# Kernel optimization log

Measured on AMD Instinct MI355X. Metric: run time of the kernel, lower is better.

## Reference

```python
import jax, jax.numpy as jnp
import numpy as np
from jax.scipy.special import ndtr

EPS1 = 1e-6
WEIGHT_DECAY = 1e-5  # FLAGS.weight_decay


def setup_inputs() -> dict:
    key = jax.random.key(0)
    ks = jax.random.split(key, 12)
    B, F, C, Z, S = 512, 512, 500, 64, 100  # batch, features, classes (r_dim), z_dim, n_sample
    lim = np.sqrt(6.0 / (C + Z))
    def glorot(k, shape):
        fan_in, fan_out = shape
        s = np.sqrt(2.0 / (fan_in + fan_out))
        return jax.random.normal(k, shape, jnp.float32) * s
    return {
        "input_X": jax.random.normal(ks[0], (B, F), jnp.float32),
        "input_Y": (jax.random.uniform(ks[1], (B, C)) < 0.1).astype(jnp.float32),  # multi-label targets
        "noise": jax.random.normal(ks[2], (S, B, Z), jnp.float32),
        "W1": glorot(ks[3], (F, 128)), "b1": jnp.zeros((128,), jnp.float32),
        "W2": glorot(ks[4], (128, 256)), "b2": jnp.zeros((256,), jnp.float32),
        "W3": glorot(ks[5], (256, 256)), "b3": jnp.zeros((256,), jnp.float32),
        "Wmu": glorot(ks[6], (256, C)), "bmu": jnp.zeros((C,), jnp.float32),
        "r_sqrt_sigma": jax.random.uniform(ks[7], (C, Z), jnp.float32, -lim, lim),
    }


def reference(input_X, input_Y, noise, W1, b1, W2, b2, W3, b3, Wmu, bmu, r_sqrt_sigma):
    # MLP trunk
    h = jax.nn.relu(input_X @ W1 + b1)
    h = jax.nn.relu(h @ W2 + b2)
    feature = jax.nn.relu(h @ W3 + b3)

    # low-rank covariance: sigma = R R^T, covariance = sigma + I
    cov_diag = jnp.sum(r_sqrt_sigma * r_sqrt_sigma, axis=1) + 1.0  # [C]

    normalized_mu = feature @ Wmu + bmu            # [B, C]
    r_mu = normalized_mu * jnp.sqrt(cov_diag)      # [B, C]

    # MC samples of latent r: [S, B, C]
    sample_r = jnp.einsum('sbz,cz->sbc', noise, r_sqrt_sigma) + r_mu

    E = ndtr(sample_r) * (1.0 - EPS1) + EPS1 * 0.5  # probit CDF, clamped
    # logprob = sum_c [ Y*log(E) + (1-Y)*log(1-E) ]  (== -sum sample_nll)
    logprob = jnp.sum(jnp.log(E) * input_Y + jnp.log1p(-E) * (1.0 - input_Y), axis=2)  # [S, B]
    maxlogprob = jnp.max(logprob, axis=0)                       # [B]
    Eprob = jnp.mean(jnp.exp(logprob - maxlogprob), axis=0)     # [B]
    nll_loss = jnp.mean(-jnp.log(Eprob) - maxlogprob)

    # marginal (independent) probit approximated by scaled sigmoid
    indiv_prob = jax.nn.sigmoid(normalized_mu * 1.70169) * (1.0 - EPS1) + 0.5 * EPS1
    cross_entropy = jnp.log(indiv_prob) * input_Y + jnp.log1p(-indiv_prob) * (1.0 - input_Y)
    marginal_loss = -jnp.mean(jnp.sum(cross_entropy, axis=1))

    l2_loss = WEIGHT_DECAY * (jnp.sum(W1 * W1) + jnp.sum(W2 * W2)
                              + jnp.sum(W3 * W3) + jnp.sum(Wmu * Wmu))
    total_loss = l2_loss + nll_loss
    return indiv_prob, nll_loss, marginal_loss, l2_loss, total_loss
```

## Files before the change

### kernel.cpp

```cpp
#include <hip/hip_runtime.h>
#include <cstddef>

#define EPS1f 1e-6f
#define WDf   1e-5f

constexpr int Bsz = 512, Csz = 500, Zsz = 64, Ssz = 100;

typedef short bf16x8 __attribute__((ext_vector_type(8)));
typedef float f32x4 __attribute__((ext_vector_type(4)));

__device__ inline short f2bf(float f) {
  union { float f; unsigned u; } v; v.f = f;
  unsigned r = (v.u + 0x7fffu + ((v.u >> 16) & 1u)) >> 16;
  return (short)r;
}

__device__ inline float log_probit(float t) {
  const float u = t * -0.70710678118654752f;
  const float au = fabsf(u);
  const float s = 1.f / fmaf(0.3275911f, au, 1.f);
  float p = fmaf(1.061405429f, s, -1.453152027f);
  p = fmaf(p, s, 1.421413741f);
  p = fmaf(p, s, -0.284496736f);
  p = fmaf(p, s, 0.254829592f);
  p = p * s;
  const float e = __expf(-au * au);
  const float f = p * e;
  const float erfc_u = (u < 0.f) ? (2.f - f) : f;
  const float E = fmaf(0.5f * erfc_u, 1.f - EPS1f, 0.5f * EPS1f);
  return __logf(E);
}

__device__ inline float block_reduce_sum(float v, float* red) {
  #pragma unroll
  for (int off = 32; off > 0; off >>= 1) v += __shfl_down(v, off, 64);
  const int lane = threadIdx.x & 63, wid = threadIdx.x >> 6;
  if (lane == 0) red[wid] = v;
  __syncthreads();
  float r = 0.f;
  if (threadIdx.x == 0) {
    const int nw = blockDim.x >> 6;
    for (int i = 0; i < nw; ++i) r += red[i];
  }
  __syncthreads();
  return r;
}

__device__ __forceinline__ void gemm32_body(
    const float* __restrict__ A, const float* __restrict__ W,
    const float* __restrict__ bias, float* __restrict__ out,
    int M, int N, int K, int bn0, int bm0, float* As_, float* Ws_, bool relu) {
  const int tid = threadIdx.x;
  const int bn = bn0 * 32, bm = bm0 * 32;
  const int sm = tid >> 3, sk4 = (tid & 7) * 4;
  const int sk = tid >> 3, sn4 = (tid & 7) * 4;
  const int tn = tid & 15, tm = tid >> 4;
  #define AS_(b, k, m) As_[(b) * 1152 + (k) * 36 + (m)]
  #define WS_(b, k, n) Ws_[(b) * 1152 + (k) * 36 + (n)]
  auto loadW = [&](int kt, float4& wv) {
    const float* wrow = W + (size_t)(kt + sk) * N;
    const int nn = bn + sn4;
    if (nn + 3 < N) wv = *reinterpret_cast<const float4*>(wrow + nn);
    else {
      wv.x = (nn + 0 < N) ? wrow[nn + 0] : 0.f;
      wv.y = (nn + 1 < N) ? wrow[nn + 1] : 0.f;
      wv.z = (nn + 2 < N) ? wrow[nn + 2] : 0.f;
      wv.w = (nn + 3 < N) ? wrow[nn + 3] : 0.f;
    }
  };
  {
    float4 av = *reinterpret_cast<const float4*>(A + (size_t)(bm + sm) * K + sk4);
    float4 wv; loadW(0, wv);
    AS_(0, sk4 + 0, sm) = av.x; AS_(0, sk4 + 1, sm) = av.y;
    AS_(0, sk4 + 2, sm) = av.z; AS_(0, sk4 + 3, sm) = av.w;
    *reinterpret_cast<float4*>(&WS_(0, sk, sn4)) = wv;
  }
  __syncthreads();
  float acc[2][2] = {};
  int pb = 0;
  for (int kt = 0; kt < K; kt += 32) {
    const bool more = (kt + 32) < K;
    float4 av2, wv2;
    if (more) {
      av2 = *reinterpret_cast<const float4*>(A + (size_t)(bm + sm) * K + kt + 32 + sk4);
      loadW(kt + 32, wv2);
    }
    #pragma unroll
    for (int k = 0; k < 32; ++k) {
      const float2 a = *reinterpret_cast<const float2*>(&AS_(pb, k, tm * 2));
      const float2 w = *reinterpret_cast<const float2*>(&WS_(pb, k, tn * 2));
      acc[0][0] = fmaf(a.x, w.x, acc[0][0]);
      acc[0][1] = fmaf(a.x, w.y, acc[0][1]);
      acc[1][0] = fmaf(a.y, w.x, acc[1][0]);
      acc[1][1] = fmaf(a.y, w.y, acc[1][1]);
    }
    if (more) {
      const int nb = pb ^ 1;
      AS_(nb, sk4 + 0, sm) = av2.x; AS_(nb, sk4 + 1, sm) = av2.y;
      AS_(nb, sk4 + 2, sm) = av2.z; AS_(nb, sk4 + 3, sm) = av2.w;
      *reinterpret_cast<float4*>(&WS_(nb, sk, sn4)) = wv2;
      __syncthreads();
      pb = nb;
    }
  }
  #pragma unroll
  for (int j = 0; j < 2; ++j) {
    const int n = bn + tn * 2 + j;
    if (n >= N) continue;
    const float bv = bias[n];
    #pragma unroll
    for (int i = 0; i < 2; ++i) {
      const int m = bm + tm * 2 + i;
      float v = acc[i][j] + bv;
      if (relu) v = fmaxf(v, 0.f);
      out[(size_t)m * N + n] = v;
    }
  }
  #undef AS_
  #undef WS_
}

__global__ __launch_bounds__(256) void prep_kernel(
    const float* __restrict__ noise, short* __restrict__ nfB,
    const float* __restrict__ R, short* __restrict__ Rb, float* __restrict__ sqrtcov,
    const float* __restrict__ X, const float* __restrict__ W1,
    const float* __restrict__ b1, float* __restrict__ h1,
    const float* __restrict__ W2, const float* __restrict__ W3,
    const float* __restrict__ Wmu, float* __restrict__ l2_part) {
  __shared__ float smem[2304 * 2];
  const int blk = blockIdx.x;
  const int tid = threadIdx.x;
  if (blk < 800) {
    const int g = blk * 256 + tid;
    const int s = g >> 11;
    const int r = g & 2047;
    const int bt = r >> 6;
    const int ln = r & 63;
    const int cl = ln & 15, grp = ln >> 4;
    const float* src = noise + ((size_t)(s * 512 + bt * 16 + cl) * 64 + grp * 8);
    const float4 a = *reinterpret_cast<const float4*>(src);
    const float4 b = *reinterpret_cast<const float4*>(src + 4);
    const float4 c = *reinterpret_cast<const float4*>(src + 32);
    const float4 d = *reinterpret_cast<const float4*>(src + 36);
    bf16x8* dst = reinterpret_cast<bf16x8*>(nfB);
    const int u = (s * 32 + bt) * 128 + ln;
    dst[u]      = bf16x8{ f2bf(a.x), f2bf(a.y), f2bf(a.z), f2bf(a.w),
                          f2bf(b.x), f2bf(b.y), f2bf(b.z), f2bf(b.w) };
    dst[u + 64] = bf16x8{ f2bf(c.x), f2bf(c.y), f2bf(c.z), f2bf(c.w),
                          f2bf(d.x), f2bf(d.y), f2bf(d.z), f2bf(d.w) };
  } else if (blk < 808) {
    const int idx = (blk - 800) * 256 + tid;
    const int c = idx >> 2;
    const int zq = (idx & 3) * 16;
    const bool cv = c < Csz;
    const float* src = R + (size_t)c * Zsz + zq;
    float4 r0, r1, r2, r3;
    if (cv) {
      r0 = *reinterpret_cast<const float4*>(src);
      r1 = *reinterpret_cast<const float4*>(src + 4);
      r2 = *reinterpret_cast<const float4*>(src + 8);
      r3 = *reinterpret_cast<const float4*>(src + 12);
    } else {
      r0 = r1 = r2 = r3 = make_float4(0.f, 0.f, 0.f, 0.f);
    }
    float ss = 0.f;
    ss = fmaf(r0.x, r0.x, ss); ss = fmaf(r0.y, r0.y, ss);
    ss = fmaf(r0.z, r0.z, ss); ss = fmaf(r0.w, r0.w, ss);
    ss = fmaf(r1.x, r1.x, ss); ss = fmaf(r1.y, r1.y, ss);
    ss = fmaf(r1.z, r1.z, ss); ss = fmaf(r1.w, r1.w, ss);
    ss = fmaf(r2.x, r2.x, ss); ss = fmaf(r2.y, r2.y, ss);
    ss = fmaf(r2.z, r2.z, ss); ss = fmaf(r2.w, r2.w, ss);
    ss = fmaf(r3.x, r3.x, ss); ss = fmaf(r3.y, r3.y, ss);
    ss = fmaf(r3.z, r3.z, ss); ss = fmaf(r3.w, r3.w, ss);
    short* dst = Rb + (size_t)c * Zsz + zq;
    *reinterpret_cast<bf16x8*>(dst) =
        bf16x8{ f2bf(r0.x), f2bf(r0.y), f2bf(r0.z), f2bf(r0.w),
                f2bf(r1.x), f2bf(r1.y), f2bf(r1.z), f2bf(r1.w) };
    *reinterpret_cast<bf16x8*>(dst + 8) =
        bf16x8{ f2bf(r2.x), f2bf(r2.y), f2bf(r2.z), f2bf(r2.w),
                f2bf(r3.x), f2bf(r3.y), f2bf(r3.z), f2bf(r3.w) };
    ss += __shfl_xor(ss, 1, 64);
    ss += __shfl_xor(ss, 2, 64);
    if ((idx & 3) == 0 && cv) sqrtcov[c] = sqrtf(1.f + ss);
  } else if (blk < 872) {
    const int bid = blk - 808;
    const int gid = bid * 256 + tid;
    const int stride = 64 * 256;
    float s = 0.f;
    for (int i = gid; i < 65536; i += stride) { float v = W1[i]; s = fmaf(v, v, s); }
    for (int i = gid; i < 32768; i += stride) { float v = W2[i]; s = fmaf(v, v, s); }
    for (int i = gid; i < 65536; i += stride) { float v = W3[i]; s = fmaf(v, v, s); }
    for (int i = gid; i < 128000; i += stride) { float v = Wmu[i]; s = fmaf(v, v, s); }
    const float tot = block_reduce_sum(s, smem);
    if (tid == 0) l2_part[bid] = tot;
  } else {
    const int idx = blk - 872;
    gemm32_body(X, W1, b1, h1, 512, 128, 512, idx & 3, idx >> 2,
                smem, smem + 2304, true);
  }
}

template <bool RELU>
__global__ __launch_bounds__(256) void gemm32(
    const float* __restrict__ A, const float* __restrict__ W,
    const float* __restrict__ bias, float* __restrict__ out,
    int M, int N, int K) {
  __shared__ float smem[2304 * 2];
  gemm32_body(A, W, bias, out, M, N, K, blockIdx.x, blockIdx.y,
              smem, smem + 2304, RELU);
}

__global__ __launch_bounds__(256) void gemm32_mu(
    const float* __restrict__ A, const float* __restrict__ W,
    const float* __restrict__ bias, const float* __restrict__ Y,
    const float* __restrict__ sqrtcov,
    float* __restrict__ out_prob, float* __restrict__ rmuB, float* __restrict__ yB,
    float* __restrict__ ce_part, int M, int N, int K) {
  __shared__ float As[2][32][36];
  __shared__ float Ws[2][32][36];
  const int tid = threadIdx.x;
  const int bn = blockIdx.x * 32, bm = blockIdx.y * 32;
  const int sm = tid >> 3, sk4 = (tid & 7) * 4;
  const int sk = tid >> 3, sn4 = (tid & 7) * 4;
  const int tn = tid & 15, tm = tid >> 4;

  auto loadW = [&](int kt, float4& wv) {
    const float* wrow = W + (size_t)(kt + sk) * N;
    const int nn = bn + sn4;
    if (nn + 3 < N) wv = *reinterpret_cast<const float4*>(wrow + nn);
    else {
      wv.x = (nn + 0 < N) ? wrow[nn + 0] : 0.f;
      wv.y = (nn + 1 < N) ? wrow[nn + 1] : 0.f;
      wv.z = (nn + 2 < N) ? wrow[nn + 2] : 0.f;
      wv.w = (nn + 3 < N) ? wrow[nn + 3] : 0.f;
    }
  };
  {
    float4 av = *reinterpret_cast<const float4*>(A + (size_t)(bm + sm) * K + sk4);
    float4 wv; loadW(0, wv);
    As[0][sk4 + 0][sm] = av.x; As[0][sk4 + 1][sm] = av.y;
    As[0][sk4 + 2][sm] = av.z; As[0][sk4 + 3][sm] = av.w;
    *reinterpret_cast<float4*>(&Ws[0][sk][sn4]) = wv;
  }
  __syncthreads();
  float acc[2][2] = {};
  int pb = 0;
  for (int kt = 0; kt < K; kt += 32) {
    const bool more = (kt + 32) < K;
    float4 av2, wv2;
    if (more) {
      av2 = *reinterpret_cast<const float4*>(A + (size_t)(bm + sm) * K + kt + 32 + sk4);
      loadW(kt + 32, wv2);
    }
    #pragma unroll
    for (int k = 0; k < 32; ++k) {
      const float2 a = *reinterpret_cast<const float2*>(&As[pb][k][tm * 2]);
      const float2 w = *reinterpret_cast<const float2*>(&Ws[pb][k][tn * 2]);
      acc[0][0] = fmaf(a.x, w.x, acc[0][0]);
      acc[0][1] = fmaf(a.x, w.y, acc[0][1]);
      acc[1][0] = fmaf(a.y, w.x, acc[1][0]);
      acc[1][1] = fmaf(a.y, w.y, acc[1][1]);
    }
    if (more) {
      const int nb = pb ^ 1;
      As[nb][sk4 + 0][sm] = av2.x; As[nb][sk4 + 1][sm] = av2.y;
      As[nb][sk4 + 2][sm] = av2.z; As[nb][sk4 + 3][sm] = av2.w;
      *reinterpret_cast<float4*>(&Ws[nb][sk][sn4]) = wv2;
      __syncthreads();
      pb = nb;
    }
  }
  float ce2[2] = {0.f, 0.f};
  #pragma unroll
  for (int i = 0; i < 2; ++i) {
    const int m = bm + tm * 2 + i;
    #pragma unroll
    for (int j = 0; j < 2; ++j) {
      const int n = bn + tn * 2 + j;
      if (n < N) {
        const float v = acc[i][j] + bias[n];
        const float sp = 1.f / (1.f + __expf(-1.70169f * v));
        const float p = fmaf(sp, 1.f - EPS1f, 0.5f * EPS1f);
        const float q = fmaf(1.f - sp, 1.f - EPS1f, 0.5f * EPS1f);
        const float y = Y[(size_t)m * N + n];
        out_prob[(size_t)m * N + n] = p;
        ce2[i] += __logf((y > 0.5f) ? p : q);
        rmuB[(size_t)m * 512 + n] = v * sqrtcov[n];
        yB[(size_t)m * 512 + n] = y;
      }
    }
  }
  #pragma unroll
  for (int off = 1; off < 16; off <<= 1) {
    ce2[0] += __shfl_xor(ce2[0], off, 64);
    ce2[1] += __shfl_xor(ce2[1], off, 64);
  }
  if (tn == 0) {
    const int m0 = bm + tm * 2;
    ce_part[(size_t)blockIdx.x * Bsz + m0] = ce2[0];
    ce_part[(size_t)blockIdx.x * Bsz + m0 + 1] = ce2[1];
  }
}

__global__ __launch_bounds__(256, 5) void logprob_s(
    const short* __restrict__ nfB, const short* __restrict__ Rb,
    const float* __restrict__ rmuB, const float* __restrict__ yB,
    float* __restrict__ lp_part) {
  const int blk = blockIdx.x;
  const int bt = blk & 31;
  const int ctg = (blk >> 5) & 7;
  const int sg = blk >> 8;
  const int wid = threadIdx.x >> 6;
  const int lane = threadIdx.x & 63;
  const int cl = lane & 15, grp = lane >> 4;
  const int ct = ctg * 4 + wid;
  const int c0 = ct * 16, b0 = bt * 16;

  const bf16x8 Rf0 = *reinterpret_cast<const bf16x8*>(Rb + (size_t)(c0 + cl) * 64 + grp * 8);
  const bf16x8 Rf1 = *reinterpret_cast<const bf16x8*>(Rb + (size_t)(c0 + cl) * 64 + 32 + grp * 8);
  const int cb = c0 + grp * 4;
  const float4 rmu4 = *reinterpret_cast<const float4*>(rmuB + (size_t)(b0 + cl) * 512 + cb);
  const float4 y4   = *reinterpret_cast<const float4*>(yB + (size_t)(b0 + cl) * 512 + cb);
  const float sn0 = fmaf(2.f, y4.x, -1.f), sn1 = fmaf(2.f, y4.y, -1.f);
  const float sn2 = fmaf(2.f, y4.z, -1.f), sn3 = fmaf(2.f, y4.w, -1.f);
  const bool v0 = cb + 0 < Csz, v1 = cb + 1 < Csz, v2 = cb + 2 < Csz, v3 = cb + 3 < Csz;

  const bf16x8* nf = reinterpret_cast<const bf16x8*>(nfB);
  const int sbase = sg * 10;
  int base = (sbase * 32 + bt) * 128 + lane;

  bf16x8 fa0 = nf[base],        fa1 = nf[base + 64];
  bf16x8 fb0 = nf[base + 4096], fb1 = nf[base + 4096 + 64];

  #pragma unroll 1
  for (int i = 0; i < 10; i += 2) {
    bf16x8 na0, na1, nb0, nb1;
    if (i < 8) {
      na0 = nf[base + 8192];  na1 = nf[base + 8192 + 64];
      nb0 = nf[base + 12288]; nb1 = nf[base + 12288 + 64];
    }
    f32x4 accA = {0.f, 0.f, 0.f, 0.f};
    f32x4 accB = {0.f, 0.f, 0.f, 0.f};
    accA = __builtin_amdgcn_mfma_f32_16x16x32_bf16(Rf0, fa0, accA, 0, 0, 0);
    accB = __builtin_amdgcn_mfma_f32_16x16x32_bf16(Rf0, fb0, accB, 0, 0, 0);
    accA = __builtin_amdgcn_mfma_f32_16x16x32_bf16(Rf1, fa1, accA, 0, 0, 0);
    accB = __builtin_amdgcn_mfma_f32_16x16x32_bf16(Rf1, fb1, accB, 0, 0, 0);
    float lpA = 0.f, lpB = 0.f;
    lpA += v0 ? log_probit((accA[0] + rmu4.x) * sn0) : 0.f;
    lpB += v0 ? log_probit((accB[0] + rmu4.x) * sn0) : 0.f;
    lpA += v1 ? log_probit((accA[1] + rmu4.y) * sn1) : 0.f;
    lpB += v1 ? log_probit((accB[1] + rmu4.y) * sn1) : 0.f;
    lpA += v2 ? log_probit((accA[2] + rmu4.z) * sn2) : 0.f;
    lpB += v2 ? log_probit((accB[2] + rmu4.z) * sn2) : 0.f;
    lpA += v3 ? log_probit((accA[3] + rmu4.w) * sn3) : 0.f;
    lpB += v3 ? log_probit((accB[3] + rmu4.w) * sn3) : 0.f;
    lpA += __shfl_xor(lpA, 16, 64);
    lpA += __shfl_xor(lpA, 32, 64);
    lpB += __shfl_xor(lpB, 16, 64);
    lpB += __shfl_xor(lpB, 32, 64);
    if (lane < 16) {
      const int s = sbase + i;
      lp_part[(size_t)(s * 32 + ct) * 512 + b0 + lane] = lpA;
      lp_part[(size_t)((s + 1) * 32 + ct) * 512 + b0 + lane] = lpB;
    }
    base += 8192;
    fa0 = na0; fa1 = na1; fb0 = nb0; fb1 = nb1;
  }
}

__global__ __launch_bounds__(256) void ctsum(const float* __restrict__ lp_part,
                                             float* __restrict__ lp_sum) {
  const int i = blockIdx.x * 256 + threadIdx.x;
  const int s = i >> 9, b = i & 511;
  const float* p = lp_part + (size_t)s * 16384 + b;
  float a0 = 0.f, a1 = 0.f, a2 = 0.f, a3 = 0.f;
  #pragma unroll
  for (int ct = 0; ct < 32; ct += 4) {
    a0 += p[(ct + 0) * 512];
    a1 += p[(ct + 1) * 512];
    a2 += p[(ct + 2) * 512];
    a3 += p[(ct + 3) * 512];
  }
  lp_sum[i] = (a0 + a1) + (a2 + a3);
}

__global__ __launch_bounds__(256) void nll_kernel(const float* __restrict__ lp_sum,
                                                  float* __restrict__ nll_b) {
  __shared__ float sm[4][64], sse[4][64];
  const int bl = threadIdx.x & 63;
  const int sc = threadIdx.x >> 6;
  const int b = blockIdx.x * 64 + bl;
  float m = -3.0e38f, se = 0.f;
  for (int s = sc * 25; s < sc * 25 + 25; ++s) {
    const float v = lp_sum[(size_t)s * Bsz + b];
    const float mn = fmaxf(m, v);
    se = se * __expf(m - mn) + __expf(v - mn);
    m = mn;
  }
  sm[sc][bl] = m; sse[sc][bl] = se;
  __syncthreads();
  if (sc == 0) {
    float M = sm[0][bl];
    #pragma unroll
    for (int i = 1; i < 4; ++i) M = fmaxf(M, sm[i][bl]);
    float SE = 0.f;
    #pragma unroll
    for (int i = 0; i < 4; ++i) SE += sse[i][bl] * __expf(sm[i][bl] - M);
    nll_b[b] = -__logf(SE * (1.f / (float)Ssz)) - M;
  }
}

__global__ __launch_bounds__(256) void finals_kernel(
    const float* __restrict__ nll_b, const float* __restrict__ ce_part,
    const float* __restrict__ l2_part, int nparts, float* __restrict__ out4) {
  __shared__ float red[4];
  const int t = threadIdx.x;
  const float snll = block_reduce_sum(nll_b[t] + nll_b[t + 256], red);
  float ce = 0.f;
  #pragma unroll
  for (int i = 0; i < 32; ++i) ce += ce_part[i * 256 + t];
  const float sce = block_reduce_sum(ce, red);
  const float sl2 = block_reduce_sum((t < nparts) ? l2_part[t] : 0.f, red);
  if (t == 0) {
    const float nll = snll / (float)Bsz;
    const float marg = -sce / (float)Bsz;
    const float l2v = WDf * sl2;
    out4[0] = nll;
    out4[1] = marg;
    out4[2] = l2v;
    out4[3] = l2v + nll;
  }
}

extern "C" void kernel_launch(void* const* d_in, const int* in_sizes, int n_in,
                              void* d_out, int out_size, void* d_ws, size_t ws_size,
                              hipStream_t stream) {
  const float* X = (const float*)d_in[0];
  const float* Y = (const float*)d_in[1];
  const float* noise = (const float*)d_in[2];
  const float* W1 = (const float*)d_in[3];
  const float* b1 = (const float*)d_in[4];
  const float* W2 = (const float*)d_in[5];
  const float* b2 = (const float*)d_in[6];
  const float* W3 = (const float*)d_in[7];
  const float* b3 = (const float*)d_in[8];
  const float* Wmu = (const float*)d_in[9];
  const float* bmu = (const float*)d_in[10];
  const float* rss = (const float*)d_in[11];

  float* ws = (float*)d_ws;
  float* lp_part = ws;
  float* h1 = ws;
  float* h2 = h1 + 65536;
  float* feat = h2 + 131072;
  float* B0 = ws + 1638400;
  float* sqrtcov = B0;
  float* rmuB = sqrtcov + 512;
  float* yB = rmuB + 262144;
  float* ce_part = yB + 262144;
  float* nll_b = ce_part + 8192;
  float* l2_part = nll_b + 512;
  float* lp_sum = l2_part + 128;
  short* Rb = (short*)(lp_sum + 51200);
  short* nfB = (short*)(lp_sum + 51200 + 16384);

  float* out_prob = (float*)d_out;
  float* out4 = out_prob + (size_t)Bsz * Csz;

  prep_kernel<<<dim3(936), 256, 0, stream>>>(noise, nfB, rss, Rb, sqrtcov,
                                             X, W1, b1, h1, W2, W3, Wmu, l2_part);

  gemm32<true><<<dim3(8, 16), 256, 0, stream>>>(h1, W2, b2, h2, 512, 256, 128);
  gemm32<true><<<dim3(8, 16), 256, 0, stream>>>(h2, W3, b3, feat, 512, 256, 256);
  gemm32_mu<<<dim3(16, 16), 256, 0, stream>>>(feat, Wmu, bmu, Y, sqrtcov,
                                              out_prob, rmuB, yB, ce_part, 512, 500, 256);

  logprob_s<<<dim3(2560), 256, 0, stream>>>(nfB, Rb, rmuB, yB, lp_part);
  ctsum<<<dim3(200), 256, 0, stream>>>(lp_part, lp_sum);
  nll_kernel<<<dim3(8), 256, 0, stream>>>(lp_sum, nll_b);

  finals_kernel<<<dim3(1), 256, 0, stream>>>(nll_b, ce_part, l2_part, 64, out4);
}
```

Measured before the change: 86.69 us.

## Fuse trunk GEMMs and tail reductions into persistent kernels with atomic grid barriers

Merges the three trunk GEMM launches into one 256-block kernel that separates phases with global atomic-counter barriers. It also merges ctsum, nll and finals into one tail kernel using arrive and wait counters. The aim is to remove per-kernel launch gaps and dependency latency between small kernels. The barriers assume every block is co-resident, which holds for 256 blocks on this GPU, and they add spin-wait and fence overhead.

Result: slower. 171.8 us (+98.2%).

```diff
diff --git a/kernel.cpp b/kernel.cpp
--- a/kernel.cpp
+++ b/kernel.cpp
@@ -44,6 +44,19 @@
   }
   __syncthreads();
   return r;
+}
+
+__device__ __forceinline__ void phase_arrive(unsigned* cnt) {
+  __threadfence();
+  __syncthreads();
+  if (threadIdx.x == 0) atomicAdd(cnt, 1u);
+}
+__device__ __forceinline__ void phase_wait(unsigned* cnt, unsigned target) {
+  if (threadIdx.x == 0) {
+    while (__hip_atomic_load(cnt, __ATOMIC_ACQUIRE, __HIP_MEMORY_SCOPE_AGENT) < target)
+      __builtin_amdgcn_s_sleep(1);
+  }
+  __syncthreads();
 }
 
 __device__ __forceinline__ void gemm32_body(
@@ -120,16 +133,112 @@
   #undef WS_
 }
 
+__device__ __forceinline__ void mu_body(
+    const float* __restrict__ A, const float* __restrict__ W,
+    const float* __restrict__ bias, const float* __restrict__ Y,
+    const float* __restrict__ sqrtcov,
+    float* __restrict__ out_prob, float* __restrict__ rmuB, float* __restrict__ yB,
+    float* __restrict__ ce_part, int bn0, int bm0, float* As_, float* Ws_) {
+  const int N = Csz, K = 256;
+  const int tid = threadIdx.x;
+  const int bn = bn0 * 32, bm = bm0 * 32;
+  const int sm = tid >> 3, sk4 = (tid & 7) * 4;
+  const int sk = tid >> 3, sn4 = (tid & 7) * 4;
+  const int tn = tid & 15, tm = tid >> 4;
+  #define AS_(b, k, m) As_[(b) * 1152 + (k) * 36 + (m)]
+  #define WS_(b, k, n) Ws_[(b) * 1152 + (k) * 36 + (n)]
+  auto loadW = [&](int kt, float4& wv) {
+    const float* wrow = W + (size_t)(kt + sk) * N;
+    const int nn = bn + sn4;
+    if (nn + 3 < N) wv = *reinterpret_cast<const float4*>(wrow + nn);
+    else {
+      wv.x = (nn + 0 < N) ? wrow[nn + 0] : 0.f;
+      wv.y = (nn + 1 < N) ? wrow[nn + 1] : 0.f;
+      wv.z = (nn + 2 < N) ? wrow[nn + 2] : 0.f;
+      wv.w = (nn + 3 < N) ? wrow[nn + 3] : 0.f;
+    }
+  };
+  {
+    float4 av = *reinterpret_cast<const float4*>(A + (size_t)(bm + sm) * K + sk4);
+    float4 wv; loadW(0, wv);
+    AS_(0, sk4 + 0, sm) = av.x; AS_(0, sk4 + 1, sm) = av.y;
+    AS_(0, sk4 + 2, sm) = av.z; AS_(0, sk4 + 3, sm) = av.w;
+    *reinterpret_cast<float4*>(&WS_(0, sk, sn4)) = wv;
+  }
+  __syncthreads();
+  float acc[2][2] = {};
+  int pb = 0;
+  for (int kt = 0; kt < K; kt += 32) {
+    const bool more = (kt + 32) < K;
+    float4 av2, wv2;
+    if (more) {
+      av2 = *reinterpret_cast<const float4*>(A + (size_t)(bm + sm) * K + kt + 32 + sk4);
+      loadW(kt + 32, wv2);
+    }
+    #pragma unroll
+    for (int k = 0; k < 32; ++k) {
+      const float2 aa = *reinterpret_cast<const float2*>(&AS_(pb, k, tm * 2));
+      const float2 ww = *reinterpret_cast<const float2*>(&WS_(pb, k, tn * 2));
+      acc[0][0] = fmaf(aa.x, ww.x, acc[0][0]);
+      acc[0][1] = fmaf(aa.x, ww.y, acc[0][1]);
+      acc[1][0] = fmaf(aa.y, ww.x, acc[1][0]);
+      acc[1][1] = fmaf(aa.y, ww.y, acc[1][1]);
+    }
+    if (more) {
+      const int nb = pb ^ 1;
+      AS_(nb, sk4 + 0, sm) = av2.x; AS_(nb, sk4 + 1, sm) = av2.y;
+      AS_(nb, sk4 + 2, sm) = av2.z; AS_(nb, sk4 + 3, sm) = av2.w;
+      *reinterpret_cast<float4*>(&WS_(nb, sk, sn4)) = wv2;
+      __syncthreads();
+      pb = nb;
+    }
+  }
+  float ce2[2] = {0.f, 0.f};
+  #pragma unroll
+  for (int i = 0; i < 2; ++i) {
+    const int m = bm + tm * 2 + i;
+    #pragma unroll
+    for (int j = 0; j < 2; ++j) {
+      const int n = bn + tn * 2 + j;
+      if (n < N) {
+        const float v = acc[i][j] + bias[n];
+        const float sp = 1.f / (1.f + __expf(-1.70169f * v));
+        const float p = fmaf(sp, 1.f - EPS1f, 0.5f * EPS1f);
+        const float q = fmaf(1.f - sp, 1.f - EPS1f, 0.5f * EPS1f);
+        const float y = Y[(size_t)m * N + n];
+        out_prob[(size_t)m * N + n] = p;
+        ce2[i] += __logf((y > 0.5f) ? p : q);
+        rmuB[(size_t)m * 512 + n] = v * sqrtcov[n];
+        yB[(size_t)m * 512 + n] = y;
+      }
+    }
+  }
+  #pragma unroll
+  for (int off = 1; off < 16; off <<= 1) {
+    ce2[0] += __shfl_xor(ce2[0], off, 64);
+    ce2[1] += __shfl_xor(ce2[1], off, 64);
+  }
+  if (tn == 0) {
+    const int m0 = bm + tm * 2;
+    ce_part[(size_t)bn0 * Bsz + m0] = ce2[0];
+    ce_part[(size_t)bn0 * Bsz + m0 + 1] = ce2[1];
+  }
+  #undef AS_
+  #undef WS_
+}
+
 __global__ __launch_bounds__(256) void prep_kernel(
     const float* __restrict__ noise, short* __restrict__ nfB,
     const float* __restrict__ R, short* __restrict__ Rb, float* __restrict__ sqrtcov,
     const float* __restrict__ X, const float* __restrict__ W1,
     const float* __restrict__ b1, float* __restrict__ h1,
     const float* __restrict__ W2, const float* __restrict__ W3,
-    const float* __restrict__ Wmu, float* __restrict__ l2_part) {
+    const float* __restrict__ Wmu, float* __restrict__ l2_part,
+    unsigned* __restrict__ cnt) {
   __shared__ float smem[2304 * 2];
   const int blk = blockIdx.x;
   const int tid = threadIdx.x;
+  if (blk == 0 && tid < 8) cnt[tid] = 0;
   if (blk < 800) {
     const int g = blk * 256 + tid;
     const int s = g >> 11;
@@ -200,106 +309,25 @@
   }
 }
 
-template <bool RELU>
-__global__ __launch_bounds__(256) void gemm32(
-    const float* __restrict__ A, const float* __restrict__ W,
-    const float* __restrict__ bias, float* __restrict__ out,
-    int M, int N, int K) {
+__global__ __launch_bounds__(256) void trunk_kernel(
+    const float* __restrict__ h1, const float* __restrict__ W2, const float* __restrict__ b2,
+    float* __restrict__ h2, const float* __restrict__ W3, const float* __restrict__ b3,
+    float* __restrict__ feat, const float* __restrict__ Wmu, const float* __restrict__ bmu,
+    const float* __restrict__ Y, const float* __restrict__ sqrtcov,
+    float* __restrict__ out_prob, float* __restrict__ rmuB, float* __restrict__ yB,
+    float* __restrict__ ce_part, unsigned* __restrict__ cnt) {
   __shared__ float smem[2304 * 2];
-  gemm32_body(A, W, bias, out, M, N, K, blockIdx.x, blockIdx.y,
-              smem, smem + 2304, RELU);
-}
-
-__global__ __launch_bounds__(256) void gemm32_mu(
-    const float* __restrict__ A, const float* __restrict__ W,
-    const float* __restrict__ bias, const float* __restrict__ Y,
-    const float* __restrict__ sqrtcov,
-    float* __restrict__ out_prob, float* __restrict__ rmuB, float* __restrict__ yB,
-    float* __restrict__ ce_part, int M, int N, int K) {
-  __shared__ float As[2][32][36];
-  __shared__ float Ws[2][32][36];
-  const int tid = threadIdx.x;
-  const int bn = blockIdx.x * 32, bm = blockIdx.y * 32;
-  const int sm = tid >> 3, sk4 = (tid & 7) * 4;
-  const int sk = tid >> 3, sn4 = (tid & 7) * 4;
-  const int tn = tid & 15, tm = tid >> 4;
-
-  auto loadW = [&](int kt, float4& wv) {
-    const float* wrow = W + (size_t)(kt + sk) * N;
-    const int nn = bn + sn4;
-    if (nn + 3 < N) wv = *reinterpret_cast<const float4*>(wrow + nn);
-    else {
-      wv.x = (nn + 0 < N) ? wrow[nn + 0] : 0.f;
-      wv.y = (nn + 1 < N) ? wrow[nn + 1] : 0.f;
-      wv.z = (nn + 2 < N) ? wrow[nn + 2] : 0.f;
-      wv.w = (nn + 3 < N) ? wrow[nn + 3] : 0.f;
-    }
-  };
-  {
-    float4 av = *reinterpret_cast<const float4*>(A + (size_t)(bm + sm) * K + sk4);
-    float4 wv; loadW(0, wv);
-    As[0][sk4 + 0][sm] = av.x; As[0][sk4 + 1][sm] = av.y;
-    As[0][sk4 + 2][sm] = av.z; As[0][sk4 + 3][sm] = av.w;
-    *reinterpret_cast<float4*>(&Ws[0][sk][sn4]) = wv;
-  }
-  __syncthreads();
-  float acc[2][2] = {};
-  int pb = 0;
-  for (int kt = 0; kt < K; kt += 32) {
-    const bool more = (kt + 32) < K;
-    float4 av2, wv2;
-    if (more) {
-      av2 = *reinterpret_cast<const float4*>(A + (size_t)(bm + sm) * K + kt + 32 + sk4);
-      loadW(kt + 32, wv2);
-    }
-    #pragma unroll
-    for (int k = 0; k < 32; ++k) {
-      const float2 a = *reinterpret_cast<const float2*>(&As[pb][k][tm * 2]);
-      const float2 w = *reinterpret_cast<const float2*>(&Ws[pb][k][tn * 2]);
-      acc[0][0] = fmaf(a.x, w.x, acc[0][0]);
-      acc[0][1] = fmaf(a.x, w.y, acc[0][1]);
-      acc[1][0] = fmaf(a.y, w.x, acc[1][0]);
-      acc[1][1] = fmaf(a.y, w.y, acc[1][1]);
-    }
-    if (more) {
-      const int nb = pb ^ 1;
-      As[nb][sk4 + 0][sm] = av2.x; As[nb][sk4 + 1][sm] = av2.y;
-      As[nb][sk4 + 2][sm] = av2.z; As[nb][sk4 + 3][sm] = av2.w;
-      *reinterpret_cast<float4*>(&Ws[nb][sk][sn4]) = wv2;
-      __syncthreads();
-      pb = nb;
-    }
-  }
-  float ce2[2] = {0.f, 0.f};
-  #pragma unroll
-  for (int i = 0; i < 2; ++i) {
-    const int m = bm + tm * 2 + i;
-    #pragma unroll
-    for (int j = 0; j < 2; ++j) {
-      const int n = bn + tn * 2 + j;
-      if (n < N) {
-        const float v = acc[i][j] + bias[n];
-        const float sp = 1.f / (1.f + __expf(-1.70169f * v));
-        const float p = fmaf(sp, 1.f - EPS1f, 0.5f * EPS1f);
-        const float q = fmaf(1.f - sp, 1.f - EPS1f, 0.5f * EPS1f);
-        const float y = Y[(size_t)m * N + n];
-        out_prob[(size_t)m * N + n] = p;
-        ce2[i] += __logf((y > 0.5f) ? p : q);
-        rmuB[(size_t)m * 512 + n] = v * sqrtcov[n];
-        yB[(size_t)m * 512 + n] = y;
-      }
-    }
-  }
-  #pragma unroll
-  for (int off = 1; off < 16; off <<= 1) {
-    ce2[0] += __shfl_xor(ce2[0], off, 64);
-    ce2[1] += __shfl_xor(ce2[1], off, 64);
-  }
-  if (tn == 0) {
-    const int m0 = bm + tm * 2;
-    ce_part[(size_t)blockIdx.x * Bsz + m0] = ce2[0];
-    ce_part[(size_t)blockIdx.x * Bsz + m0 + 1] = ce2[1];
-  }
+  const int bid = (int)blockIdx.x;
+  if (bid < 128)
+    gemm32_body(h1, W2, b2, h2, 512, 256, 128, bid & 7, bid >> 3, smem, smem + 2304, true);
+  phase_arrive(cnt + 0);
+  phase_wait(cnt + 0, 256);
+  if (bid < 128)
+    gemm32_body(h2, W3, b3, feat, 512, 256, 256, bid & 7, bid >> 3, smem, smem + 2304, true);
+  phase_arrive(cnt + 1);
+  phase_wait(cnt + 1, 256);
+  mu_body(feat, Wmu, bmu, Y, sqrtcov, out_prob, rmuB, yB, ce_part,
+          bid & 15, bid >> 4, smem, smem + 2304);
 }
 
 __global__ __launch_bounds__(256, 5) void logprob_s(
@@ -368,67 +396,79 @@
   }
 }
 
-__global__ __launch_bounds__(256) void ctsum(const float* __restrict__ lp_part,
-                                             float* __restrict__ lp_sum) {
-  const int i = blockIdx.x * 256 + threadIdx.x;
-  const int s = i >> 9, b = i & 511;
-  const float* p = lp_part + (size_t)s * 16384 + b;
-  float a0 = 0.f, a1 = 0.f, a2 = 0.f, a3 = 0.f;
-  #pragma unroll
-  for (int ct = 0; ct < 32; ct += 4) {
-    a0 += p[(ct + 0) * 512];
-    a1 += p[(ct + 1) * 512];
-    a2 += p[(ct + 2) * 512];
-    a3 += p[(ct + 3) * 512];
-  }
-  lp_sum[i] = (a0 + a1) + (a2 + a3);
-}
-
-__global__ __launch_bounds__(256) void nll_kernel(const float* __restrict__ lp_sum,
-                                                  float* __restrict__ nll_b) {
-  __shared__ float sm[4][64], sse[4][64];
-  const int bl = threadIdx.x & 63;
-  const int sc = threadIdx.x >> 6;
-  const int b = blockIdx.x * 64 + bl;
-  float m = -3.0e38f, se = 0.f;
-  for (int s = sc * 25; s < sc * 25 + 25; ++s) {
-    const float v = lp_sum[(size_t)s * Bsz + b];
-    const float mn = fmaxf(m, v);
-    se = se * __expf(m - mn) + __expf(v - mn);
-    m = mn;
-  }
-  sm[sc][bl] = m; sse[sc][bl] = se;
-  __syncthreads();
-  if (sc == 0) {
-    float M = sm[0][bl];
+__global__ __launch_bounds__(256) void tail_kernel(
+    const float* __restrict__ lp_part, float* __restrict__ lp_sum,
+    float* __restrict__ nll_b, const float* __restrict__ ce_part,
+    const float* __restrict__ l2_part, float* __restrict__ out4,
+    unsigned* __restrict__ cnt) {
+  __shared__ float tsm[520];
+  const int bid = (int)blockIdx.x;
+  const int tid = (int)threadIdx.x;
+
+  {
+    const int i = bid * 256 + tid;
+    const int s = i >> 9, b = i & 511;
+    const float* p = lp_part + (size_t)s * 16384 + b;
+    float a0 = 0.f, a1 = 0.f, a2 = 0.f, a3 = 0.f;
     #pragma unroll
-    for (int i = 1; i < 4; ++i) M = fmaxf(M, sm[i][bl]);
-    float SE = 0.f;
+    for (int ct = 0; ct < 32; ct += 4) {
+      a0 += p[(ct + 0) * 512];
+      a1 += p[(ct + 1) * 512];
+      a2 += p[(ct + 2) * 512];
+      a3 += p[(ct + 3) * 512];
+    }
+    lp_sum[i] = (a0 + a1) + (a2 + a3);
+  }
+  phase_arrive(cnt + 2);
+  if (bid >= 8) return;
+  phase_wait(cnt + 2, 200);
+
+  {
+    float* sm = tsm;
+    float* sse = tsm + 256;
+    const int bl = tid & 63;
+    const int sc = tid >> 6;
+    const int b = bid * 64 + bl;
+    float m = -3.0e38f, se = 0.f;
+    for (int s = sc * 25; s < sc * 25 + 25; ++s) {
+      const float v = lp_sum[(size_t)s * Bsz + b];
+      const float mn = fmaxf(m, v);
+      se = se * __expf(m - mn) + __expf(v - mn);
+      m = mn;
+    }
+    sm[sc * 64 + bl] = m; sse[sc * 64 + bl] = se;
+    __syncthreads();
+    if (sc == 0) {
+      float M = sm[bl];
+      #pragma unroll
+      for (int i = 1; i < 4; ++i) M = fmaxf(M, sm[i * 64 + bl]);
+      float SE = 0.f;
+      #pragma unroll
+      for (int i = 0; i < 4; ++i) SE += sse[i * 64 + bl] * __expf(sm[i * 64 + bl] - M);
+      nll_b[b] = -__logf(SE * (1.f / (float)Ssz)) - M;
+    }
+  }
+  phase_arrive(cnt + 3);
+  if (bid != 0) return;
+  phase_wait(cnt + 3, 8);
+
+  {
+    float* red = tsm + 512;
+    const float snll = block_reduce_sum(nll_b[tid] + nll_b[tid + 256], red);
+    float ce = 0.f;
     #pragma unroll
-    for (int i = 0; i < 4; ++i) SE += sse[i][bl] * __expf(sm[i][bl] - M);
-    nll_b[b] = -__logf(SE * (1.f / (float)Ssz)) - M;
-  }
-}
-
-__global__ __launch_bounds__(256) void finals_kernel(
-    const float* __restrict__ nll_b, const float* __restrict__ ce_part,
-    const float* __restrict__ l2_part, int nparts, float* __restrict__ out4) {
-  __shared__ float red[4];
-  const int t = threadIdx.x;
-  const float snll = block_reduce_sum(nll_b[t] + nll_b[t + 256], red);
-  float ce = 0.f;
-  #pragma unroll
-  for (int i = 0; i < 32; ++i) ce += ce_part[i * 256 + t];
-  const float sce = block_reduce_sum(ce, red);
-  const float sl2 = block_reduce_sum((t < nparts) ? l2_part[t] : 0.f, red);
-  if (t == 0) {
-    const float nll = snll / (float)Bsz;
-    const float marg = -sce / (float)Bsz;
-    const float l2v = WDf * sl2;
-    out4[0] = nll;
-    out4[1] = marg;
-    out4[2] = l2v;
-    out4[3] = l2v + nll;
+    for (int i = 0; i < 32; ++i) ce += ce_part[i * 256 + tid];
+    const float sce = block_reduce_sum(ce, red);
+    const float sl2 = block_reduce_sum((tid < 64) ? l2_part[tid] : 0.f, red);
+    if (tid == 0) {
+      const float nll = snll / (float)Bsz;
+      const float marg = -sce / (float)Bsz;
+      const float l2v = WDf * sl2;
+      out4[0] = nll;
+      out4[1] = marg;
+      out4[2] = l2v;
+      out4[3] = l2v + nll;
+    }
   }
 }
 
@@ -462,22 +502,20 @@
   float* l2_part = nll_b + 512;
   float* lp_sum = l2_part + 128;
   short* Rb = (short*)(lp_sum + 51200);
-  short* nfB = (short*)(lp_sum + 51200 + 16384);
+  short* nfB = Rb + 32768;
+  unsigned* cnt = (unsigned*)(nfB + 3276800);
 
   float* out_prob = (float*)d_out;
   float* out4 = out_prob + (size_t)Bsz * Csz;
 
   prep_kernel<<<dim3(936), 256, 0, stream>>>(noise, nfB, rss, Rb, sqrtcov,
-                                             X, W1, b1, h1, W2, W3, Wmu, l2_part);
-
-  gemm32<true><<<dim3(8, 16), 256, 0, stream>>>(h1, W2, b2, h2, 512, 256, 128);
-  gemm32<true><<<dim3(8, 16), 256, 0, stream>>>(h2, W3, b3, feat, 512, 256, 256);
-  gemm32_mu<<<dim3(16, 16), 256, 0, stream>>>(feat, Wmu, bmu, Y, sqrtcov,
-                                              out_prob, rmuB, yB, ce_part, 512, 500, 256);
+                                             X, W1, b1, h1, W2, W3, Wmu, l2_part, cnt);
+
+  trunk_kernel<<<dim3(256), 256, 0, stream>>>(h1, W2, b2, h2, W3, b3, feat, Wmu, bmu,
+                                              Y, sqrtcov, out_prob, rmuB, yB, ce_part, cnt);
 
   logprob_s<<<dim3(2560), 256, 0, stream>>>(nfB, Rb, rmuB, yB, lp_part);
-  ctsum<<<dim3(200), 256, 0, stream>>>(lp_part, lp_sum);
-  nll_kernel<<<dim3(8), 256, 0, stream>>>(lp_sum, nll_b);
-
-  finals_kernel<<<dim3(1), 256, 0, stream>>>(nll_b, ce_part, l2_part, 64, out4);
-}
+
+  tail_kernel<<<dim3(200), 256, 0, stream>>>(lp_part, lp_sum, nll_b, ce_part,
+                                             l2_part, out4, cnt);
+}
```
